# Kernel tuning notes

Hardware: AMD Instinct MI355X
Metric: run time of the kernel (lower is better)

The kernel has to match this reference:

```python
import jax, jax.numpy as jnp
import numpy as np

NUM_TAGS = 3


def setup_inputs() -> dict:
    key = jax.random.key(0)
    k1, k2, k3 = jax.random.split(key, 3)
    B, T, K = 2048, 4096, NUM_TAGS
    logits = jax.random.normal(k1, (B, T, K), dtype=jnp.float32)
    transitions = jax.random.normal(k2, (K, K), dtype=jnp.float32)
    tags = jax.random.randint(k3, (B, T), 0, K, dtype=jnp.int64)
    return {"logits": logits, "transitions": transitions, "tags": tags}


def reference(logits, transitions, tags):
    """Negative CRF log-likelihood (AllenNLP CRF, include_start_end_transitions=False,
    full mask), i.e. -(sum_b [joint_score(b) - log_partition(b)])."""
    # --- log partition via forward algorithm (lax.scan over time) ---
    # alpha: [B, K]; emissions scanned over time: [T-1, B, K]
    def step(alpha, emit_t):
        # broadcast: alpha[b, i] + transitions[i, j] -> logsumexp over i
        new_alpha = jax.nn.logsumexp(alpha[:, :, None] + transitions[None, :, :], axis=1) + emit_t
        return new_alpha, None

    alpha0 = logits[:, 0, :]                              # [B, K]
    emits_rest = jnp.swapaxes(logits[:, 1:, :], 0, 1)     # [T-1, B, K]
    alpha_T, _ = jax.lax.scan(step, alpha0, emits_rest)
    log_z = jax.nn.logsumexp(alpha_T, axis=1)             # [B]

    # --- joint (numerator) score of the gold tag sequence ---
    emit_score = jnp.take_along_axis(logits, tags[:, :, None], axis=2)[..., 0].sum(axis=1)  # [B]
    trans_score = transitions[tags[:, :-1], tags[:, 1:]].sum(axis=1)                         # [B]

    loglik = emit_score + trans_score - log_z
    return -jnp.sum(loglik)
```

## Files before the change

kernel.cpp:

```cpp
#include <hip/hip_runtime.h>

#define BB 2048
#define TT 4096
#define LN2 0.69314718055994530942f

__global__ __launch_bounds__(256, 5) void crf_pass1(
    const float* __restrict__ logits, const float* __restrict__ trans,
    const int* __restrict__ tags, float* __restrict__ ws)
{
    __shared__ float sTrans[9];
    __shared__ float sTrExp[9];
    __shared__ float sRec[3][12];
    const int tid = threadIdx.x;
    if (tid < 9) {
        float tv = trans[tid];
        sTrans[tid] = tv;
        sTrExp[tid] = __expf(tv);
    }
    __syncthreads();

    const int b = blockIdx.x;
    const int c = tid;

    const int4*   tp = (const int4*)(tags + (size_t)b * TT + (size_t)c * 16);
    const float4* lp = (const float4*)(logits + ((size_t)b * TT + (size_t)c * 16) * 3);

    int4 Tq[4];
#pragma unroll
    for (int i = 0; i < 4; ++i) Tq[i] = tp[i];
    float Lf[48];
#pragma unroll
    for (int i = 0; i < 12; ++i) {
        float4 t = lp[i];
        Lf[4*i+0] = t.x; Lf[4*i+1] = t.y; Lf[4*i+2] = t.z; Lf[4*i+3] = t.w;
    }
    __builtin_amdgcn_sched_barrier(0);

    unsigned pk = 0;
#pragma unroll
    for (int i = 0; i < 4; ++i) {
        pk |= ((unsigned)Tq[i].x << (8*i))     | ((unsigned)Tq[i].y << (8*i+2))
            | ((unsigned)Tq[i].z << (8*i+4))   | ((unsigned)Tq[i].w << (8*i+6));
    }

    float t00 = sTrExp[0], t01 = sTrExp[1], t02 = sTrExp[2];
    float t10 = sTrExp[3], t11 = sTrExp[4], t12 = sTrExp[5];
    float t20 = sTrExp[6], t21 = sTrExp[7], t22 = sTrExp[8];

    float a00 = 1.f, a01 = 0.f, a02 = 0.f;
    float a10 = 0.f, a11 = 1.f, a12 = 0.f;
    float a20 = 0.f, a21 = 0.f, a22 = 1.f;
    int   se = 0;
    float score = 0.f;
    unsigned long long acc = 0ull;
    int prev = 0;

#define MATSTEP(e0_, e1_, e2_) do {                                     \
    float x0 = __expf(e0_), x1 = __expf(e1_), x2 = __expf(e2_);         \
    float b0 = (a00*t00 + a01*t10 + a02*t20) * x0;                      \
    float b1 = (a00*t01 + a01*t11 + a02*t21) * x1;                      \
    float b2 = (a00*t02 + a01*t12 + a02*t22) * x2;                      \
    float b3 = (a10*t00 + a11*t10 + a12*t20) * x0;                      \
    float b4 = (a10*t01 + a11*t11 + a12*t21) * x1;                      \
    float b5 = (a10*t02 + a11*t12 + a12*t22) * x2;                      \
    float b6 = (a20*t00 + a21*t10 + a22*t20) * x0;                      \
    float b7 = (a20*t01 + a21*t11 + a22*t21) * x1;                      \
    float b8 = (a20*t02 + a21*t12 + a22*t22) * x2;                      \
    a00=b0; a01=b1; a02=b2; a10=b3; a11=b4; a12=b5; a20=b6; a21=b7; a22=b8; \
} while (0)

#define RENORM do {                                                     \
    float m_ = fmaxf(fmaxf(fmaxf(a00, a01), fmaxf(a02, a10)),           \
                     fmaxf(fmaxf(a11, a12), fmaxf(fmaxf(a20, a21), a22))); \
    int ef_ = (int)(__float_as_uint(m_) >> 23);                         \
    float scf_ = __uint_as_float((unsigned)(254 - ef_) << 23);          \
    se += ef_ - 127;                                                    \
    a00 *= scf_; a01 *= scf_; a02 *= scf_;                              \
    a10 *= scf_; a11 *= scf_; a12 *= scf_;                              \
    a20 *= scf_; a21 *= scf_; a22 *= scf_;                              \
} while (0)

#pragma unroll
    for (int s = 0; s < 16; ++s) {
        float e0 = Lf[3*s+0], e1 = Lf[3*s+1], e2 = Lf[3*s+2];
        int tg = (int)((pk >> (2*s)) & 3u);
        if (s == 0) {
            if (c != 0) MATSTEP(e0, e1, e2);
        } else {
            MATSTEP(e0, e1, e2);
            acc += 1ull << (7 * (prev * 3 + tg));
        }
        score += (tg == 0) ? e0 : ((tg == 1) ? e1 : e2);
        prev = tg;
        if ((s & 7) == 7) RENORM;
    }

    int firstTag = (int)(pk & 3u);

#pragma unroll
    for (int p = 0; p < 9; ++p)
        score += (float)((int)((acc >> (7 * p)) & 127ull)) * sTrans[p];

#pragma unroll
    for (int m = 1; m < 64; m <<= 1) {
        float o00 = __shfl_down(a00, m, 64), o01 = __shfl_down(a01, m, 64), o02 = __shfl_down(a02, m, 64);
        float o10 = __shfl_down(a10, m, 64), o11 = __shfl_down(a11, m, 64), o12 = __shfl_down(a12, m, 64);
        float o20 = __shfl_down(a20, m, 64), o21 = __shfl_down(a21, m, 64), o22 = __shfl_down(a22, m, 64);
        int   ose = __shfl_down(se, m, 64);
        float osc = __shfl_down(score, m, 64);
        int   ofi = __shfl_down(firstTag, m, 64);
        int   opv = __shfl_down(prev, m, 64);

        float c00 = a00*o00 + a01*o10 + a02*o20;
        float c01 = a00*o01 + a01*o11 + a02*o21;
        float c02 = a00*o02 + a01*o12 + a02*o22;
        float c10 = a10*o00 + a11*o10 + a12*o20;
        float c11 = a10*o01 + a11*o11 + a12*o21;
        float c12 = a10*o02 + a11*o12 + a12*o22;
        float c20 = a20*o00 + a21*o10 + a22*o20;
        float c21 = a20*o01 + a21*o11 + a22*o21;
        float c22 = a20*o02 + a21*o12 + a22*o22;

        score = score + osc + sTrans[prev * 3 + ofi];
        prev = opv;
        se += ose;

        a00=c00; a01=c01; a02=c02; a10=c10; a11=c11; a12=c12; a20=c20; a21=c21; a22=c22;
        RENORM;
    }

    const int lane = tid & 63;
    const int wid  = tid >> 6;
    if (lane == 0 && wid > 0) {
        sRec[wid-1][0] = a00; sRec[wid-1][1] = a01; sRec[wid-1][2] = a02;
        sRec[wid-1][3] = a10; sRec[wid-1][4] = a11; sRec[wid-1][5] = a12;
        sRec[wid-1][6] = a20; sRec[wid-1][7] = a21; sRec[wid-1][8] = a22;
        sRec[wid-1][9]  = __int_as_float(se);
        sRec[wid-1][10] = score;
        sRec[wid-1][11] = __int_as_float(firstTag | (prev << 8));
    }
    __syncthreads();
    if (tid == 0) {
#pragma unroll
        for (int k = 0; k < 3; ++k) {
            float m00 = sRec[k][0], m01 = sRec[k][1], m02 = sRec[k][2];
            float m10 = sRec[k][3], m11 = sRec[k][4], m12 = sRec[k][5];
            float m20 = sRec[k][6], m21 = sRec[k][7], m22 = sRec[k][8];
            int   shm = __float_as_int(sRec[k][9]);
            float scm = sRec[k][10];
            int   pkm = __float_as_int(sRec[k][11]);

            float c00 = a00*m00 + a01*m10 + a02*m20;
            float c01 = a00*m01 + a01*m11 + a02*m21;
            float c02 = a00*m02 + a01*m12 + a02*m22;
            float c10 = a10*m00 + a11*m10 + a12*m20;
            float c11 = a10*m01 + a11*m11 + a12*m21;
            float c12 = a10*m02 + a11*m12 + a12*m22;
            float c20 = a20*m00 + a21*m10 + a22*m20;
            float c21 = a20*m01 + a21*m11 + a22*m21;
            float c22 = a20*m02 + a21*m12 + a22*m22;

            score += scm + sTrans[prev * 3 + (pkm & 255)];
            prev = pkm >> 8;
            se += shm;
            a00=c00; a01=c01; a02=c02; a10=c10; a11=c11; a12=c12; a20=c20; a21=c21; a22=c22;
            RENORM;
        }
        const float* lb = logits + (size_t)b * TT * 3;
        float v0 = __expf(lb[0]);
        float v1 = __expf(lb[1]);
        float v2 = __expf(lb[2]);
        float n0 = v0*a00 + v1*a10 + v2*a20;
        float n1 = v0*a01 + v1*a11 + v2*a21;
        float n2 = v0*a02 + v1*a12 + v2*a22;
        float logz = logf(n0 + n1 + n2) + (float)se * LN2;
        ws[b] = logz - score;
    }

#undef MATSTEP
#undef RENORM
}

__global__ __launch_bounds__(256) void crf_reduce(
    const float* __restrict__ ws, float* __restrict__ out)
{
    int tid = threadIdx.x;
    float s = 0.f;
#pragma unroll
    for (int k = 0; k < BB / 256; ++k) s += ws[k * 256 + tid];
    for (int off = 32; off > 0; off >>= 1) s += __shfl_down(s, off, 64);
    __shared__ float sP[4];
    if ((tid & 63) == 0) sP[tid >> 6] = s;
    __syncthreads();
    if (tid == 0) out[0] = sP[0] + sP[1] + sP[2] + sP[3];
}

extern "C" void kernel_launch(void* const* d_in, const int* in_sizes, int n_in,
                              void* d_out, int out_size, void* d_ws, size_t ws_size,
                              hipStream_t stream) {
    const float* logits = (const float*)d_in[0];
    const float* trans  = (const float*)d_in[1];
    const int*   tags   = (const int*)d_in[2];
    float* out = (float*)d_out;
    float* ws  = (float*)d_ws;

    crf_pass1<<<dim3(BB), dim3(256), 0, stream>>>(logits, trans, tags, ws);
    crf_reduce<<<dim3(1), dim3(256), 0, stream>>>(ws, out);
}
```

Before: 32.86 us.

## Split logits loads into two halves to cut registers and raise occupancy

The per-thread 48-float logits buffer becomes two 24-float halves. The second half is loaded only after the first 8 steps are done, and sched_barriers stop the compiler from hoisting that load. This lowers register pressure so the launch-bounds hint can go from 5 to 8 blocks per CU, giving more waves to hide memory latency. The cost is that the second load is serialized behind the first half's compute inside each thread, so that latency is exposed unless other waves cover it.

```diff
diff --git a/kernel.cpp b/kernel.cpp
--- a/kernel.cpp
+++ b/kernel.cpp
@@ -4,7 +4,7 @@
 #define TT 4096
 #define LN2 0.69314718055994530942f
 
-__global__ __launch_bounds__(256, 5) void crf_pass1(
+__global__ __launch_bounds__(256, 8) void crf_pass1(
     const float* __restrict__ logits, const float* __restrict__ trans,
     const int* __restrict__ tags, float* __restrict__ ws)
 {
@@ -28,11 +28,11 @@
     int4 Tq[4];
 #pragma unroll
     for (int i = 0; i < 4; ++i) Tq[i] = tp[i];
-    float Lf[48];
-#pragma unroll
-    for (int i = 0; i < 12; ++i) {
+    float Lh1[24];
+#pragma unroll
+    for (int i = 0; i < 6; ++i) {
         float4 t = lp[i];
-        Lf[4*i+0] = t.x; Lf[4*i+1] = t.y; Lf[4*i+2] = t.z; Lf[4*i+3] = t.w;
+        Lh1[4*i+0] = t.x; Lh1[4*i+1] = t.y; Lh1[4*i+2] = t.z; Lh1[4*i+3] = t.w;
     }
     __builtin_amdgcn_sched_barrier(0);
 
@@ -80,20 +80,38 @@
     a20 *= scf_; a21 *= scf_; a22 *= scf_;                              \
 } while (0)
 
-#pragma unroll
-    for (int s = 0; s < 16; ++s) {
-        float e0 = Lf[3*s+0], e1 = Lf[3*s+1], e2 = Lf[3*s+2];
-        int tg = (int)((pk >> (2*s)) & 3u);
-        if (s == 0) {
-            if (c != 0) MATSTEP(e0, e1, e2);
-        } else {
-            MATSTEP(e0, e1, e2);
-            acc += 1ull << (7 * (prev * 3 + tg));
-        }
-        score += (tg == 0) ? e0 : ((tg == 1) ? e1 : e2);
-        prev = tg;
-        if ((s & 7) == 7) RENORM;
-    }
+#define DOSTEP(s_, e0_, e1_, e2_) do {                                  \
+    int tg = (int)((pk >> (2*(s_))) & 3u);                              \
+    if ((s_) == 0) {                                                    \
+        if (c != 0) MATSTEP(e0_, e1_, e2_);                             \
+    } else {                                                            \
+        MATSTEP(e0_, e1_, e2_);                                         \
+        acc += 1ull << (7 * (prev * 3 + tg));                           \
+    }                                                                   \
+    score += (tg == 0) ? (e0_) : ((tg == 1) ? (e1_) : (e2_));           \
+    prev = tg;                                                          \
+} while (0)
+
+#pragma unroll
+    for (int s = 0; s < 8; ++s) {
+        DOSTEP(s, Lh1[3*s+0], Lh1[3*s+1], Lh1[3*s+2]);
+    }
+    RENORM;
+    __builtin_amdgcn_sched_barrier(0);
+
+    float Lh2[24];
+#pragma unroll
+    for (int i = 0; i < 6; ++i) {
+        float4 t = lp[6 + i];
+        Lh2[4*i+0] = t.x; Lh2[4*i+1] = t.y; Lh2[4*i+2] = t.z; Lh2[4*i+3] = t.w;
+    }
+    __builtin_amdgcn_sched_barrier(0);
+
+#pragma unroll
+    for (int s = 8; s < 16; ++s) {
+        DOSTEP(s, Lh2[3*(s-8)+0], Lh2[3*(s-8)+1], Lh2[3*(s-8)+2]);
+    }
+    RENORM;
 
     int firstTag = (int)(pk & 3u);
 
@@ -179,6 +197,7 @@
 
 #undef MATSTEP
 #undef RENORM
+#undef DOSTEP
 }
 
 __global__ __launch_bounds__(256) void crf_reduce(
```

After: 96.70 us. 2.94x slower.

## Process two batch rows per block and prefetch next row during reduction

Applied to the files above, without the earlier changes.

Each block now handles two sequences. The loads for the second row are issued right after the first row's serial scan, so they can overlap the shuffle and shared-memory reductions. The first-timestep exponentials are now computed in-register by thread 0 instead of being reloaded from global memory, and the tag/prev pair is packed into one shuffle. The grid shrinks by half and the occupancy hint drops from 5 to 4, which may reduce latency hiding across blocks.

```diff
diff --git a/kernel.cpp b/kernel.cpp
--- a/kernel.cpp
+++ b/kernel.cpp
@@ -3,8 +3,9 @@
 #define BB 2048
 #define TT 4096
 #define LN2 0.69314718055994530942f
-
-__global__ __launch_bounds__(256, 5) void crf_pass1(
+#define ROWS 2
+
+__global__ __launch_bounds__(256, 4) void crf_pass1(
     const float* __restrict__ logits, const float* __restrict__ trans,
     const int* __restrict__ tags, float* __restrict__ ws)
 {
@@ -19,54 +20,40 @@
     }
     __syncthreads();
 
-    const int b = blockIdx.x;
-    const int c = tid;
-
-    const int4*   tp = (const int4*)(tags + (size_t)b * TT + (size_t)c * 16);
-    const float4* lp = (const float4*)(logits + ((size_t)b * TT + (size_t)c * 16) * 3);
-
-    int4 Tq[4];
-#pragma unroll
-    for (int i = 0; i < 4; ++i) Tq[i] = tp[i];
+    const int c  = tid;
+    const int b0 = blockIdx.x * ROWS;
+
+    int4  Tq[4];
     float Lf[48];
-#pragma unroll
-    for (int i = 0; i < 12; ++i) {
-        float4 t = lp[i];
-        Lf[4*i+0] = t.x; Lf[4*i+1] = t.y; Lf[4*i+2] = t.z; Lf[4*i+3] = t.w;
+    {
+        const int4*   tp = (const int4*)(tags + (size_t)b0 * TT + (size_t)c * 16);
+        const float4* lp = (const float4*)(logits + ((size_t)b0 * TT + (size_t)c * 16) * 3);
+#pragma unroll
+        for (int i = 0; i < 4; ++i) Tq[i] = tp[i];
+#pragma unroll
+        for (int i = 0; i < 12; ++i) {
+            float4 t = lp[i];
+            Lf[4*i+0] = t.x; Lf[4*i+1] = t.y; Lf[4*i+2] = t.z; Lf[4*i+3] = t.w;
+        }
     }
     __builtin_amdgcn_sched_barrier(0);
 
-    unsigned pk = 0;
-#pragma unroll
-    for (int i = 0; i < 4; ++i) {
-        pk |= ((unsigned)Tq[i].x << (8*i))     | ((unsigned)Tq[i].y << (8*i+2))
-            | ((unsigned)Tq[i].z << (8*i+4))   | ((unsigned)Tq[i].w << (8*i+6));
-    }
-
-    float t00 = sTrExp[0], t01 = sTrExp[1], t02 = sTrExp[2];
-    float t10 = sTrExp[3], t11 = sTrExp[4], t12 = sTrExp[5];
-    float t20 = sTrExp[6], t21 = sTrExp[7], t22 = sTrExp[8];
-
-    float a00 = 1.f, a01 = 0.f, a02 = 0.f;
-    float a10 = 0.f, a11 = 1.f, a12 = 0.f;
-    float a20 = 0.f, a21 = 0.f, a22 = 1.f;
-    int   se = 0;
-    float score = 0.f;
-    unsigned long long acc = 0ull;
-    int prev = 0;
+    const float t00 = sTrExp[0], t01 = sTrExp[1], t02 = sTrExp[2];
+    const float t10 = sTrExp[3], t11 = sTrExp[4], t12 = sTrExp[5];
+    const float t20 = sTrExp[6], t21 = sTrExp[7], t22 = sTrExp[8];
 
 #define MATSTEP(e0_, e1_, e2_) do {                                     \
     float x0 = __expf(e0_), x1 = __expf(e1_), x2 = __expf(e2_);         \
-    float b0 = (a00*t00 + a01*t10 + a02*t20) * x0;                      \
-    float b1 = (a00*t01 + a01*t11 + a02*t21) * x1;                      \
-    float b2 = (a00*t02 + a01*t12 + a02*t22) * x2;                      \
-    float b3 = (a10*t00 + a11*t10 + a12*t20) * x0;                      \
-    float b4 = (a10*t01 + a11*t11 + a12*t21) * x1;                      \
-    float b5 = (a10*t02 + a11*t12 + a12*t22) * x2;                      \
-    float b6 = (a20*t00 + a21*t10 + a22*t20) * x0;                      \
-    float b7 = (a20*t01 + a21*t11 + a22*t21) * x1;                      \
-    float b8 = (a20*t02 + a21*t12 + a22*t22) * x2;                      \
-    a00=b0; a01=b1; a02=b2; a10=b3; a11=b4; a12=b5; a20=b6; a21=b7; a22=b8; \
+    float b0_ = (a00*t00 + a01*t10 + a02*t20) * x0;                     \
+    float b1_ = (a00*t01 + a01*t11 + a02*t21) * x1;                     \
+    float b2_ = (a00*t02 + a01*t12 + a02*t22) * x2;                     \
+    float b3_ = (a10*t00 + a11*t10 + a12*t20) * x0;                     \
+    float b4_ = (a10*t01 + a11*t11 + a12*t21) * x1;                     \
+    float b5_ = (a10*t02 + a11*t12 + a12*t22) * x2;                     \
+    float b6_ = (a20*t00 + a21*t10 + a22*t20) * x0;                     \
+    float b7_ = (a20*t01 + a21*t11 + a22*t21) * x1;                     \
+    float b8_ = (a20*t02 + a21*t12 + a22*t22) * x2;                     \
+    a00=b0_; a01=b1_; a02=b2_; a10=b3_; a11=b4_; a12=b5_; a20=b6_; a21=b7_; a22=b8_; \
 } while (0)
 
 #define RENORM do {                                                     \
@@ -81,100 +68,137 @@
 } while (0)
 
 #pragma unroll
-    for (int s = 0; s < 16; ++s) {
-        float e0 = Lf[3*s+0], e1 = Lf[3*s+1], e2 = Lf[3*s+2];
-        int tg = (int)((pk >> (2*s)) & 3u);
-        if (s == 0) {
-            if (c != 0) MATSTEP(e0, e1, e2);
-        } else {
-            MATSTEP(e0, e1, e2);
-            acc += 1ull << (7 * (prev * 3 + tg));
-        }
-        score += (tg == 0) ? e0 : ((tg == 1) ? e1 : e2);
-        prev = tg;
-        if ((s & 7) == 7) RENORM;
-    }
-
-    int firstTag = (int)(pk & 3u);
-
-#pragma unroll
-    for (int p = 0; p < 9; ++p)
-        score += (float)((int)((acc >> (7 * p)) & 127ull)) * sTrans[p];
-
-#pragma unroll
-    for (int m = 1; m < 64; m <<= 1) {
-        float o00 = __shfl_down(a00, m, 64), o01 = __shfl_down(a01, m, 64), o02 = __shfl_down(a02, m, 64);
-        float o10 = __shfl_down(a10, m, 64), o11 = __shfl_down(a11, m, 64), o12 = __shfl_down(a12, m, 64);
-        float o20 = __shfl_down(a20, m, 64), o21 = __shfl_down(a21, m, 64), o22 = __shfl_down(a22, m, 64);
-        int   ose = __shfl_down(se, m, 64);
-        float osc = __shfl_down(score, m, 64);
-        int   ofi = __shfl_down(firstTag, m, 64);
-        int   opv = __shfl_down(prev, m, 64);
-
-        float c00 = a00*o00 + a01*o10 + a02*o20;
-        float c01 = a00*o01 + a01*o11 + a02*o21;
-        float c02 = a00*o02 + a01*o12 + a02*o22;
-        float c10 = a10*o00 + a11*o10 + a12*o20;
-        float c11 = a10*o01 + a11*o11 + a12*o21;
-        float c12 = a10*o02 + a11*o12 + a12*o22;
-        float c20 = a20*o00 + a21*o10 + a22*o20;
-        float c21 = a20*o01 + a21*o11 + a22*o21;
-        float c22 = a20*o02 + a21*o12 + a22*o22;
-
-        score = score + osc + sTrans[prev * 3 + ofi];
-        prev = opv;
-        se += ose;
-
-        a00=c00; a01=c01; a02=c02; a10=c10; a11=c11; a12=c12; a20=c20; a21=c21; a22=c22;
-        RENORM;
-    }
-
-    const int lane = tid & 63;
-    const int wid  = tid >> 6;
-    if (lane == 0 && wid > 0) {
-        sRec[wid-1][0] = a00; sRec[wid-1][1] = a01; sRec[wid-1][2] = a02;
-        sRec[wid-1][3] = a10; sRec[wid-1][4] = a11; sRec[wid-1][5] = a12;
-        sRec[wid-1][6] = a20; sRec[wid-1][7] = a21; sRec[wid-1][8] = a22;
-        sRec[wid-1][9]  = __int_as_float(se);
-        sRec[wid-1][10] = score;
-        sRec[wid-1][11] = __int_as_float(firstTag | (prev << 8));
-    }
-    __syncthreads();
-    if (tid == 0) {
-#pragma unroll
-        for (int k = 0; k < 3; ++k) {
-            float m00 = sRec[k][0], m01 = sRec[k][1], m02 = sRec[k][2];
-            float m10 = sRec[k][3], m11 = sRec[k][4], m12 = sRec[k][5];
-            float m20 = sRec[k][6], m21 = sRec[k][7], m22 = sRec[k][8];
-            int   shm = __float_as_int(sRec[k][9]);
-            float scm = sRec[k][10];
-            int   pkm = __float_as_int(sRec[k][11]);
-
-            float c00 = a00*m00 + a01*m10 + a02*m20;
-            float c01 = a00*m01 + a01*m11 + a02*m21;
-            float c02 = a00*m02 + a01*m12 + a02*m22;
-            float c10 = a10*m00 + a11*m10 + a12*m20;
-            float c11 = a10*m01 + a11*m11 + a12*m21;
-            float c12 = a10*m02 + a11*m12 + a12*m22;
-            float c20 = a20*m00 + a21*m10 + a22*m20;
-            float c21 = a20*m01 + a21*m11 + a22*m21;
-            float c22 = a20*m02 + a21*m12 + a22*m22;
-
-            score += scm + sTrans[prev * 3 + (pkm & 255)];
-            prev = pkm >> 8;
-            se += shm;
+    for (int r = 0; r < ROWS; ++r) {
+        const int b = b0 + r;
+
+        unsigned pk = 0;
+#pragma unroll
+        for (int i = 0; i < 4; ++i) {
+            pk |= ((unsigned)Tq[i].x << (8*i))   | ((unsigned)Tq[i].y << (8*i+2))
+                | ((unsigned)Tq[i].z << (8*i+4)) | ((unsigned)Tq[i].w << (8*i+6));
+        }
+        const int firstTag = (int)(pk & 3u);
+
+        float a00 = 1.f, a01 = 0.f, a02 = 0.f;
+        float a10 = 0.f, a11 = 1.f, a12 = 0.f;
+        float a20 = 0.f, a21 = 0.f, a22 = 1.f;
+        int   se = 0;
+        float score = 0.f;
+        unsigned long long acc = 0ull;
+        int prev = 0;
+        float v0 = 0.f, v1 = 0.f, v2 = 0.f;
+
+#pragma unroll
+        for (int s = 0; s < 16; ++s) {
+            float e0 = Lf[3*s+0], e1 = Lf[3*s+1], e2 = Lf[3*s+2];
+            int tg = (int)((pk >> (2*s)) & 3u);
+            if (s == 0) {
+                if (c == 0) {
+                    v0 = __expf(e0); v1 = __expf(e1); v2 = __expf(e2);
+                } else {
+                    MATSTEP(e0, e1, e2);
+                }
+            } else {
+                MATSTEP(e0, e1, e2);
+                acc += 1ull << (7 * (prev * 3 + tg));
+            }
+            score += (tg == 0) ? e0 : ((tg == 1) ? e1 : e2);
+            prev = tg;
+            if ((s & 7) == 7) RENORM;
+        }
+
+        if (r + 1 < ROWS) {
+            const int4*   tp2 = (const int4*)(tags + (size_t)(b + 1) * TT + (size_t)c * 16);
+            const float4* lp2 = (const float4*)(logits + ((size_t)(b + 1) * TT + (size_t)c * 16) * 3);
+#pragma unroll
+            for (int i = 0; i < 4; ++i) Tq[i] = tp2[i];
+#pragma unroll
+            for (int i = 0; i < 12; ++i) {
+                float4 t = lp2[i];
+                Lf[4*i+0] = t.x; Lf[4*i+1] = t.y; Lf[4*i+2] = t.z; Lf[4*i+3] = t.w;
+            }
+        }
+        __builtin_amdgcn_sched_barrier(0);
+
+#pragma unroll
+        for (int p = 0; p < 9; ++p)
+            score += (float)((int)((acc >> (7 * p)) & 127ull)) * sTrans[p];
+
+        int fT = firstTag;
+        int fp = fT | (prev << 8);
+#pragma unroll
+        for (int m = 1; m < 64; m <<= 1) {
+            float o00 = __shfl_down(a00, m, 64), o01 = __shfl_down(a01, m, 64), o02 = __shfl_down(a02, m, 64);
+            float o10 = __shfl_down(a10, m, 64), o11 = __shfl_down(a11, m, 64), o12 = __shfl_down(a12, m, 64);
+            float o20 = __shfl_down(a20, m, 64), o21 = __shfl_down(a21, m, 64), o22 = __shfl_down(a22, m, 64);
+            int   ose = __shfl_down(se, m, 64);
+            float osc = __shfl_down(score, m, 64);
+            int   ofp = __shfl_down(fp, m, 64);
+
+            float c00 = a00*o00 + a01*o10 + a02*o20;
+            float c01 = a00*o01 + a01*o11 + a02*o21;
+            float c02 = a00*o02 + a01*o12 + a02*o22;
+            float c10 = a10*o00 + a11*o10 + a12*o20;
+            float c11 = a10*o01 + a11*o11 + a12*o21;
+            float c12 = a10*o02 + a11*o12 + a12*o22;
+            float c20 = a20*o00 + a21*o10 + a22*o20;
+            float c21 = a20*o01 + a21*o11 + a22*o21;
+            float c22 = a20*o02 + a21*o12 + a22*o22;
+
+            score = score + osc + sTrans[(fp >> 8) * 3 + (ofp & 255)];
+            fp = (fp & 255) | (ofp & ~255);
+            se += ose;
+
             a00=c00; a01=c01; a02=c02; a10=c10; a11=c11; a12=c12; a20=c20; a21=c21; a22=c22;
             RENORM;
         }
-        const float* lb = logits + (size_t)b * TT * 3;
-        float v0 = __expf(lb[0]);
-        float v1 = __expf(lb[1]);
-        float v2 = __expf(lb[2]);
-        float n0 = v0*a00 + v1*a10 + v2*a20;
-        float n1 = v0*a01 + v1*a11 + v2*a21;
-        float n2 = v0*a02 + v1*a12 + v2*a22;
-        float logz = logf(n0 + n1 + n2) + (float)se * LN2;
-        ws[b] = logz - score;
+        prev = fp >> 8;
+        fT   = fp & 255;
+
+        const int lane = tid & 63;
+        const int wid  = tid >> 6;
+        __syncthreads();
+        if (lane == 0 && wid > 0) {
+            sRec[wid-1][0] = a00; sRec[wid-1][1] = a01; sRec[wid-1][2] = a02;
+            sRec[wid-1][3] = a10; sRec[wid-1][4] = a11; sRec[wid-1][5] = a12;
+            sRec[wid-1][6] = a20; sRec[wid-1][7] = a21; sRec[wid-1][8] = a22;
+            sRec[wid-1][9]  = __int_as_float(se);
+            sRec[wid-1][10] = score;
+            sRec[wid-1][11] = __int_as_float(fT | (prev << 8));
+        }
+        __syncthreads();
+        if (tid == 0) {
+#pragma unroll
+            for (int k = 0; k < 3; ++k) {
+                float m00 = sRec[k][0], m01 = sRec[k][1], m02 = sRec[k][2];
+                float m10 = sRec[k][3], m11 = sRec[k][4], m12 = sRec[k][5];
+                float m20 = sRec[k][6], m21 = sRec[k][7], m22 = sRec[k][8];
+                int   shm = __float_as_int(sRec[k][9]);
+                float scm = sRec[k][10];
+                int   pkm = __float_as_int(sRec[k][11]);
+
+                float c00 = a00*m00 + a01*m10 + a02*m20;
+                float c01 = a00*m01 + a01*m11 + a02*m21;
+                float c02 = a00*m02 + a01*m12 + a02*m22;
+                float c10 = a10*m00 + a11*m10 + a12*m20;
+                float c11 = a10*m01 + a11*m11 + a12*m21;
+                float c12 = a10*m02 + a11*m12 + a12*m22;
+                float c20 = a20*m00 + a21*m10 + a22*m20;
+                float c21 = a20*m01 + a21*m11 + a22*m21;
+                float c22 = a20*m02 + a21*m12 + a22*m22;
+
+                score += scm + sTrans[prev * 3 + (pkm & 255)];
+                prev = pkm >> 8;
+                se += shm;
+                a00=c00; a01=c01; a02=c02; a10=c10; a11=c11; a12=c12; a20=c20; a21=c21; a22=c22;
+                RENORM;
+            }
+            float n0 = v0*a00 + v1*a10 + v2*a20;
+            float n1 = v0*a01 + v1*a11 + v2*a21;
+            float n2 = v0*a02 + v1*a12 + v2*a22;
+            float logz = logf(n0 + n1 + n2) + (float)se * LN2;
+            ws[b] = logz - score;
+        }
     }
 
 #undef MATSTEP
@@ -204,6 +228,6 @@
     float* out = (float*)d_out;
     float* ws  = (float*)d_ws;
 
-    crf_pass1<<<dim3(BB), dim3(256), 0, stream>>>(logits, trans, tags, ws);
+    crf_pass1<<<dim3(BB / ROWS), dim3(256), 0, stream>>>(logits, trans, tags, ws);
     crf_reduce<<<dim3(1), dim3(256), 0, stream>>>(ws, out);
 }
```

New measurement: 49.07 us. +49.3%, slower.
